# Kernel tuning notes

Measured on AMD Instinct MI355X. Metric: run time of the kernel, lower is better.

The kernel has to match this reference:

```python
import jax, jax.numpy as jnp
import numpy as np
import math

B, Q, K, C, H, D = 2, 2048, 2048, 512, 8, 64  # hidden_dim*num_heads == C


def setup_inputs() -> dict:
    key = jax.random.key(0)
    ks = jax.random.split(key, 9)
    s = 0.02
    return {
        "query_data": jax.random.normal(ks[0], (B, Q, C), jnp.float32),
        "key_data": jax.random.normal(ks[1], (B, K, C), jnp.float32),
        "bias1": jax.random.normal(ks[2], (B, 1, Q, K), jnp.float32),
        "bias2": jax.random.normal(ks[3], (1, H, Q, K), jnp.float32),
        "wq": jax.random.normal(ks[4], (C, H * D), jnp.float32) * s,
        "wk": jax.random.normal(ks[5], (C, H * D), jnp.float32) * s,
        "wv": jax.random.normal(ks[6], (C, H * D), jnp.float32) * s,
        "wo": jax.random.normal(ks[7], (H * D, C), jnp.float32) * s,
        "bo": jnp.zeros((C,), jnp.float32),
        "wg": jax.random.normal(ks[8], (C, H * D), jnp.float32) * s,
        "bg": jnp.zeros((H * D,), jnp.float32),
    }


def reference(query_data, key_data, bias1, bias2, wq, wk, wv, wo, bo, wg, bg):
    # prep_qkv: project, split heads, scale q by 1/sqrt(hidden_dim)
    q = (query_data @ wq).reshape(B, Q, H, D) / math.sqrt(D)
    k = (key_data @ wk).reshape(B, K, H, D)
    v = (key_data @ wv).reshape(B, K, H, D)
    # attention: scores [B,H,Q,K] with additive biases, softmax over K
    scores = jnp.einsum("bqhd,bkhd->bhqk", q, k) + bias1 + bias2
    attn = jax.nn.softmax(scores, axis=-1)
    out = jnp.einsum("bhqk,bkhd->bqhd", attn, v)  # [B,Q,H,D]
    # wrap_up: sigmoid gate from query data, flatten heads, output proj
    g = jax.nn.sigmoid(query_data @ wg + bg).reshape(B, Q, H, D)
    out = (out * g).reshape(B, Q, H * D)
    return out @ wo + bo
```

## Files before the change

### kernel.cpp

```cpp
#include <hip/hip_runtime.h>

typedef __bf16 bf16;
typedef __bf16 bf16x8 __attribute__((ext_vector_type(8)));
typedef __bf16 bf16x4 __attribute__((ext_vector_type(4)));
typedef float f32x4 __attribute__((ext_vector_type(4)));

#define NB 2
#define NQ 2048
#define NKK 2048
#define NC 512
#define NH 8
#define ND 64
#define NM (NB*NQ)
#define SPLITS 4
#define KSPL (NKK/SPLITS)
#define NTILES (KSPL/32)

__global__ __launch_bounds__(256) void cvt_bf16_kernel(const float* __restrict__ in,
                                                       bf16* __restrict__ out, int n4) {
  int i = blockIdx.x * 256 + threadIdx.x;
  if (i < n4) {
    float4 v = ((const float4*)in)[i];
    bf16x4 o;
    o[0] = (bf16)v.x; o[1] = (bf16)v.y; o[2] = (bf16)v.z; o[3] = (bf16)v.w;
    ((bf16x4*)out)[i] = o;
  }
}

__global__ __launch_bounds__(256) void transpose_w_kernel(const float* __restrict__ W,
                                                          bf16* __restrict__ WT) {
  __shared__ float t[32][33];
  int n0 = blockIdx.x * 32, k0 = blockIdx.y * 32;
  int c = threadIdx.x & 31, r0 = threadIdx.x >> 5;
  for (int r = r0; r < 32; r += 8) t[r][c] = W[(size_t)(k0 + r) * NC + n0 + c];
  __syncthreads();
  for (int r = r0; r < 32; r += 8) WT[(size_t)(n0 + r) * NC + k0 + c] = (bf16)t[c][r];
}

__global__ __launch_bounds__(256) void gemm_kernel(const bf16* __restrict__ X,
                                                   const bf16* __restrict__ WT,
                                                   const float* __restrict__ bias,
                                                   void* __restrict__ out, int epi) {
  __shared__ bf16 Xs[64][72];
  __shared__ bf16 Ws[64][72];
  int m0 = blockIdx.y * 64, n0 = blockIdx.x * 64;
  int tid = threadIdx.x, lane = tid & 63, wave = tid >> 6;
  int wm = wave >> 1, wn = wave & 1;
  int lr = lane & 15, lg = lane >> 4;
  f32x4 acc[2][2] = {};
  for (int k0 = 0; k0 < 512; k0 += 64) {
#pragma unroll
    for (int j = 0; j < 2; j++) {
      int cc = tid + 256 * j;
      int r = cc >> 3, c8 = (cc & 7) * 8;
      *(uint4*)&Xs[r][c8] = *(const uint4*)&X[(size_t)(m0 + r) * 512 + k0 + c8];
      *(uint4*)&Ws[r][c8] = *(const uint4*)&WT[(size_t)(n0 + r) * 512 + k0 + c8];
    }
    __syncthreads();
#pragma unroll
    for (int kk = 0; kk < 64; kk += 32) {
      bf16x8 a[2], b[2];
      a[0] = *(const bf16x8*)&Xs[wm * 32 + lr][kk + lg * 8];
      a[1] = *(const bf16x8*)&Xs[wm * 32 + 16 + lr][kk + lg * 8];
      b[0] = *(const bf16x8*)&Ws[wn * 32 + lr][kk + lg * 8];
      b[1] = *(const bf16x8*)&Ws[wn * 32 + 16 + lr][kk + lg * 8];
#pragma unroll
      for (int mi = 0; mi < 2; mi++)
#pragma unroll
        for (int ni = 0; ni < 2; ni++)
          acc[mi][ni] = __builtin_amdgcn_mfma_f32_16x16x32_bf16(a[mi], b[ni], acc[mi][ni], 0, 0, 0);
    }
    __syncthreads();
  }
#pragma unroll
  for (int mi = 0; mi < 2; mi++) {
#pragma unroll
    for (int ni = 0; ni < 2; ni++) {
#pragma unroll
      for (int i = 0; i < 4; i++) {
        int grow = m0 + wm * 32 + mi * 16 + lg * 4 + i;
        int gcol = n0 + wn * 32 + ni * 16 + lr;
        float v = acc[mi][ni][i];
        if (epi == 0) {
          int b = grow >> 11, q = grow & 2047, h = gcol >> 6, d = gcol & 63;
          ((bf16*)out)[((size_t)(b * NH + h) * NQ + q) * ND + d] = (bf16)(v * 0.125f);
        } else if (epi == 1 || epi == 2) {
          int b = grow >> 11, kq = grow & 2047, h = gcol >> 6, d = gcol & 63;
          ((bf16*)out)[((size_t)(b * NH + h) * NKK + kq) * ND + d] = (bf16)v;
        } else if (epi == 3) {
          v += bias[gcol];
          v = 1.0f / (1.0f + __expf(-v));
          ((float*)out)[(size_t)grow * 512 + gcol] = v;
        } else {
          ((float*)out)[(size_t)grow * 512 + gcol] = v + bias[gcol];
        }
      }
    }
  }
}

__global__ __launch_bounds__(256) void transpose_v_kernel(const bf16* __restrict__ vh,
                                                          bf16* __restrict__ vT) {
  __shared__ bf16 t[64][72];
  int bh = blockIdx.y;
  int kk0 = blockIdx.x * 64;
  const bf16* src = vh + (size_t)bh * NKK * ND;
  bf16* dst = vT + (size_t)bh * ND * NKK;
#pragma unroll
  for (int j = 0; j < 2; j++) {
    int c = threadIdx.x + 256 * j;
    int r = c >> 3, cc = (c & 7) * 8;
    *(uint4*)&t[r][cc] = *(const uint4*)&src[(size_t)(kk0 + r) * ND + cc];
  }
  __syncthreads();
#pragma unroll
  for (int j = 0; j < 2; j++) {
    int c = threadIdx.x + 256 * j;
    int d = c >> 3, ck = (c & 7) * 8;
    bf16 tmp[8];
#pragma unroll
    for (int x = 0; x < 8; x++) tmp[x] = t[ck + x][d];
    *(uint4*)&dst[(size_t)d * NKK + kk0 + ck] = *(const uint4*)tmp;
  }
}

struct Tile {
  float b1v[2][4];
  float b2v[2][4];
  bf16x8 kf[2][2];
  bf16x8 vf[4];
};

__device__ __forceinline__ void load_tile(int k0, const float* __restrict__ b1,
                                          const float* __restrict__ b2,
                                          const bf16* __restrict__ Kp,
                                          const bf16* __restrict__ Vt,
                                          int lr, int lg, Tile& T) {
#pragma unroll
  for (int f = 0; f < 2; f++) {
#pragma unroll
    for (int i = 0; i < 4; i++) {
      int row = lg * 4 + i;
      int col = k0 + f * 16 + lr;
      T.b1v[f][i] = b1[row * NKK + col];
      T.b2v[f][i] = b2[row * NKK + col];
    }
  }
#pragma unroll
  for (int f = 0; f < 2; f++) {
#pragma unroll
    for (int kc = 0; kc < 2; kc++)
      T.kf[f][kc] = *(const bf16x8*)&Kp[(size_t)(k0 + f * 16 + lr) * ND + kc * 32 + lg * 8];
  }
#pragma unroll
  for (int ni = 0; ni < 4; ni++)
    T.vf[ni] = *(const bf16x8*)&Vt[(size_t)(ni * 16 + lr) * NKK + k0 + lg * 8];
}

__device__ __forceinline__ void compute_tile(const Tile& T, bf16x8 qf0, bf16x8 qf1,
                                             f32x4 (&o)[4], float (&lrow)[4],
                                             bf16 (*pl)[36], int lr, int lg) {
  f32x4 s[2];
#pragma unroll
  for (int f = 0; f < 2; f++) {
    f32x4 c;
#pragma unroll
    for (int i = 0; i < 4; i++) c[i] = T.b1v[f][i] + T.b2v[f][i];
    c = __builtin_amdgcn_mfma_f32_16x16x32_bf16(qf0, T.kf[f][0], c, 0, 0, 0);
    c = __builtin_amdgcn_mfma_f32_16x16x32_bf16(qf1, T.kf[f][1], c, 0, 0, 0);
    s[f] = c;
  }
#pragma unroll
  for (int i = 0; i < 4; i++) {
    float p0 = __expf(s[0][i]);
    float p1 = __expf(s[1][i]);
    lrow[i] += p0 + p1;
    pl[lg * 4 + i][lr] = (bf16)p0;
    pl[lg * 4 + i][16 + lr] = (bf16)p1;
  }
  bf16x8 pa = *(const bf16x8*)&pl[lr][lg * 8];
#pragma unroll
  for (int ni = 0; ni < 4; ni++)
    o[ni] = __builtin_amdgcn_mfma_f32_16x16x32_bf16(pa, T.vf[ni], o[ni], 0, 0, 0);
}

__global__ __launch_bounds__(1024, 4) void attn_kernel(
    const bf16* __restrict__ qh, const bf16* __restrict__ kh, const bf16* __restrict__ vT,
    const float* __restrict__ bias1, const float* __restrict__ bias2,
    float* __restrict__ o_part, float* __restrict__ l_part) {
  __shared__ bf16 plds[16][16][36];
  int l = blockIdx.x;
  int swz = (l & 7) * 64 + (l >> 3);
  int q0 = (swz & 127) * 16;
  int split = swz >> 7;
  int w = threadIdx.x >> 6, lane = threadIdx.x & 63;
  int b = w >> 3, h = w & 7;
  int lr = lane & 15, lg = lane >> 4;
  int kbase = split * KSPL;
  const bf16* Qp = qh + ((size_t)(b * NH + h) * NQ + q0) * ND;
  const bf16* Kp = kh + (size_t)(b * NH + h) * NKK * ND;
  const bf16* Vt = vT + (size_t)(b * NH + h) * ND * NKK;
  const float* b1 = bias1 + ((size_t)b * NQ + q0) * NKK;
  const float* b2 = bias2 + ((size_t)h * NQ + q0) * NKK;

  bf16x8 qf0 = *(const bf16x8*)&Qp[lr * 64 + lg * 8];
  bf16x8 qf1 = *(const bf16x8*)&Qp[lr * 64 + 32 + lg * 8];

  f32x4 o[4] = {};
  float lrow[4] = {0.f, 0.f, 0.f, 0.f};
  bf16(*pl)[36] = plds[w];

  Tile T;
  for (int t = 0; t < NTILES; t++) {
    load_tile(kbase + t * 32, b1, b2, Kp, Vt, lr, lg, T);
    compute_tile(T, qf0, qf1, o, lrow, pl, lr, lg);
  }

  float lred[4];
#pragma unroll
  for (int i = 0; i < 4; i++) {
    float L = lrow[i];
    L += __shfl_xor(L, 1);
    L += __shfl_xor(L, 2);
    L += __shfl_xor(L, 4);
    L += __shfl_xor(L, 8);
    lred[i] = L;
  }

  float* op = o_part + (((size_t)(split * NB + b) * NH + h) * NQ + q0) * ND;
#pragma unroll
  for (int ni = 0; ni < 4; ni++)
#pragma unroll
    for (int i = 0; i < 4; i++)
      op[(lg * 4 + i) * ND + ni * 16 + lr] = o[ni][i];
  if (lr == 0) {
    float* lp = l_part + ((size_t)(split * NB + b) * NH + h) * NQ + q0;
#pragma unroll
    for (int i = 0; i < 4; i++) lp[lg * 4 + i] = lred[i];
  }
}

__global__ __launch_bounds__(256) void combine_kernel(const float* __restrict__ o_part,
                                                      const float* __restrict__ l_part,
                                                      const float* __restrict__ gate,
                                                      bf16* __restrict__ ao) {
  size_t t = (size_t)blockIdx.x * 256 + threadIdx.x;
  int d0 = (int)(t & 15) * 4;
  int h = (int)((t >> 4) & 7);
  int q = (int)((t >> 7) & 2047);
  int b = (int)(t >> 18);
  f32x4 acc = {};
  float L = 0.f;
#pragma unroll
  for (int s = 0; s < SPLITS; s++) {
    size_t base = (((size_t)(s * NB + b) * NH + h) * NQ + q);
    acc += *(const f32x4*)&o_part[base * ND + d0];
    L += l_part[base];
  }
  float inv = 1.0f / L;
  size_t gi = ((size_t)b * NQ + q) * 512 + h * 64 + d0;
  f32x4 g = *(const f32x4*)&gate[gi];
  bf16x4 r;
#pragma unroll
  for (int j = 0; j < 4; j++) r[j] = (bf16)(acc[j] * inv * g[j]);
  *(bf16x4*)&ao[gi] = r;
}

extern "C" void kernel_launch(void* const* d_in, const int* in_sizes, int n_in,
                              void* d_out, int out_size, void* d_ws, size_t ws_size,
                              hipStream_t stream) {
  const float* query = (const float*)d_in[0];
  const float* keyd  = (const float*)d_in[1];
  const float* bias1 = (const float*)d_in[2];
  const float* bias2 = (const float*)d_in[3];
  const float* wq = (const float*)d_in[4];
  const float* wk = (const float*)d_in[5];
  const float* wv = (const float*)d_in[6];
  const float* wo = (const float*)d_in[7];
  const float* bo = (const float*)d_in[8];
  const float* wg = (const float*)d_in[9];
  const float* bg = (const float*)d_in[10];

  char* ws = (char*)d_ws;
  size_t off = 0;
  auto alloc = [&](size_t bytes) {
    void* p = ws + off;
    off += (bytes + 255) & ~(size_t)255;
    return p;
  };
  bf16* qd_bf = (bf16*)alloc((size_t)NM * 512 * 2);
  bf16* kd_bf = (bf16*)alloc((size_t)NM * 512 * 2);
  bf16* wqT = (bf16*)alloc((size_t)512 * 512 * 2);
  bf16* wkT = (bf16*)alloc((size_t)512 * 512 * 2);
  bf16* wvT = (bf16*)alloc((size_t)512 * 512 * 2);
  bf16* wgT = (bf16*)alloc((size_t)512 * 512 * 2);
  bf16* woT = (bf16*)alloc((size_t)512 * 512 * 2);
  bf16* qh  = (bf16*)alloc((size_t)NB * NH * NQ * ND * 2);
  bf16* kh  = (bf16*)alloc((size_t)NB * NH * NKK * ND * 2);
  bf16* vh  = (bf16*)alloc((size_t)NB * NH * NKK * ND * 2);
  bf16* vTt = (bf16*)alloc((size_t)NB * NH * ND * NKK * 2);
  float* gbuf = (float*)alloc((size_t)NM * 512 * 4);
  bf16* aob = (bf16*)alloc((size_t)NM * 512 * 2);
  float* o_part = (float*)alloc((size_t)SPLITS * NB * NH * NQ * ND * 4);
  float* l_part = (float*)alloc((size_t)SPLITS * NB * NH * NQ * 4);

  int n4 = NM * 512 / 4;
  cvt_bf16_kernel<<<dim3(n4 / 256), 256, 0, stream>>>(query, qd_bf, n4);
  cvt_bf16_kernel<<<dim3(n4 / 256), 256, 0, stream>>>(keyd, kd_bf, n4);

  transpose_w_kernel<<<dim3(16, 16), 256, 0, stream>>>(wq, wqT);
  transpose_w_kernel<<<dim3(16, 16), 256, 0, stream>>>(wk, wkT);
  transpose_w_kernel<<<dim3(16, 16), 256, 0, stream>>>(wv, wvT);
  transpose_w_kernel<<<dim3(16, 16), 256, 0, stream>>>(wg, wgT);
  transpose_w_kernel<<<dim3(16, 16), 256, 0, stream>>>(wo, woT);

  gemm_kernel<<<dim3(8, 64), 256, 0, stream>>>(qd_bf, wqT, nullptr, qh, 0);
  gemm_kernel<<<dim3(8, 64), 256, 0, stream>>>(kd_bf, wkT, nullptr, kh, 1);
  gemm_kernel<<<dim3(8, 64), 256, 0, stream>>>(kd_bf, wvT, nullptr, vh, 2);
  gemm_kernel<<<dim3(8, 64), 256, 0, stream>>>(qd_bf, wgT, bg, gbuf, 3);

  transpose_v_kernel<<<dim3(32, 16), 256, 0, stream>>>(vh, vTt);

  attn_kernel<<<dim3(512), 1024, 0, stream>>>(qh, kh, vTt, bias1, bias2, o_part, l_part);

  combine_kernel<<<dim3((NB * NQ * NH * 16) / 256), 256, 0, stream>>>(o_part, l_part, gbuf, aob);

  gemm_kernel<<<dim3(8, 64), 256, 0, stream>>>(aob, woT, bo, d_out, 4);
}
```

Baseline: 258.7 us.

## Transpose QK^T mfma so bias loads vectorize, and prefetch bias tiles ahead

Swaps the operands of the score MFMA so each lane holds four consecutive key columns for one query row. The bias1/bias2 reads then become 16-byte float4 loads instead of scattered scalar loads. Bias tiles are double-buffered one tile ahead in a fully unrolled loop. The probability writes to LDS become packed bf16x4 stores with a padded stride of 40, and the row-sum reduction shrinks to two shuffles. Register pressure rises from the unrolling and prefetch, which could hurt occupancy at the 1024-thread launch bound.

```diff
diff --git a/kernel.cpp b/kernel.cpp
--- a/kernel.cpp
+++ b/kernel.cpp
@@ -15,6 +15,7 @@
 #define SPLITS 4
 #define KSPL (NKK/SPLITS)
 #define NTILES (KSPL/32)
+#define PLS 40
 
 __global__ __launch_bounds__(256) void cvt_bf16_kernel(const float* __restrict__ in,
                                                        bf16* __restrict__ out, int n4) {
@@ -124,71 +125,11 @@
   }
 }
 
-struct Tile {
-  float b1v[2][4];
-  float b2v[2][4];
-  bf16x8 kf[2][2];
-  bf16x8 vf[4];
-};
-
-__device__ __forceinline__ void load_tile(int k0, const float* __restrict__ b1,
-                                          const float* __restrict__ b2,
-                                          const bf16* __restrict__ Kp,
-                                          const bf16* __restrict__ Vt,
-                                          int lr, int lg, Tile& T) {
-#pragma unroll
-  for (int f = 0; f < 2; f++) {
-#pragma unroll
-    for (int i = 0; i < 4; i++) {
-      int row = lg * 4 + i;
-      int col = k0 + f * 16 + lr;
-      T.b1v[f][i] = b1[row * NKK + col];
-      T.b2v[f][i] = b2[row * NKK + col];
-    }
-  }
-#pragma unroll
-  for (int f = 0; f < 2; f++) {
-#pragma unroll
-    for (int kc = 0; kc < 2; kc++)
-      T.kf[f][kc] = *(const bf16x8*)&Kp[(size_t)(k0 + f * 16 + lr) * ND + kc * 32 + lg * 8];
-  }
-#pragma unroll
-  for (int ni = 0; ni < 4; ni++)
-    T.vf[ni] = *(const bf16x8*)&Vt[(size_t)(ni * 16 + lr) * NKK + k0 + lg * 8];
-}
-
-__device__ __forceinline__ void compute_tile(const Tile& T, bf16x8 qf0, bf16x8 qf1,
-                                             f32x4 (&o)[4], float (&lrow)[4],
-                                             bf16 (*pl)[36], int lr, int lg) {
-  f32x4 s[2];
-#pragma unroll
-  for (int f = 0; f < 2; f++) {
-    f32x4 c;
-#pragma unroll
-    for (int i = 0; i < 4; i++) c[i] = T.b1v[f][i] + T.b2v[f][i];
-    c = __builtin_amdgcn_mfma_f32_16x16x32_bf16(qf0, T.kf[f][0], c, 0, 0, 0);
-    c = __builtin_amdgcn_mfma_f32_16x16x32_bf16(qf1, T.kf[f][1], c, 0, 0, 0);
-    s[f] = c;
-  }
-#pragma unroll
-  for (int i = 0; i < 4; i++) {
-    float p0 = __expf(s[0][i]);
-    float p1 = __expf(s[1][i]);
-    lrow[i] += p0 + p1;
-    pl[lg * 4 + i][lr] = (bf16)p0;
-    pl[lg * 4 + i][16 + lr] = (bf16)p1;
-  }
-  bf16x8 pa = *(const bf16x8*)&pl[lr][lg * 8];
-#pragma unroll
-  for (int ni = 0; ni < 4; ni++)
-    o[ni] = __builtin_amdgcn_mfma_f32_16x16x32_bf16(pa, T.vf[ni], o[ni], 0, 0, 0);
-}
-
 __global__ __launch_bounds__(1024, 4) void attn_kernel(
     const bf16* __restrict__ qh, const bf16* __restrict__ kh, const bf16* __restrict__ vT,
     const float* __restrict__ bias1, const float* __restrict__ bias2,
     float* __restrict__ o_part, float* __restrict__ l_part) {
-  __shared__ bf16 plds[16][16][36];
+  __shared__ bf16 plds[16][16][PLS];
   int l = blockIdx.x;
   int swz = (l & 7) * 64 + (l >> 3);
   int q0 = (swz & 127) * 16;
@@ -198,34 +139,75 @@
   int lr = lane & 15, lg = lane >> 4;
   int kbase = split * KSPL;
   const bf16* Qp = qh + ((size_t)(b * NH + h) * NQ + q0) * ND;
-  const bf16* Kp = kh + (size_t)(b * NH + h) * NKK * ND;
-  const bf16* Vt = vT + (size_t)(b * NH + h) * ND * NKK;
-  const float* b1 = bias1 + ((size_t)b * NQ + q0) * NKK;
-  const float* b2 = bias2 + ((size_t)h * NQ + q0) * NKK;
+  const bf16* Kp = kh + (size_t)(b * NH + h) * NKK * ND + (size_t)kbase * ND;
+  const bf16* Vt = vT + (size_t)(b * NH + h) * ND * NKK + kbase;
+  const float* b1p = bias1 + ((size_t)b * NQ + q0 + lr) * NKK + kbase + lg * 4;
+  const float* b2p = bias2 + ((size_t)h * NQ + q0 + lr) * NKK + kbase + lg * 4;
 
   bf16x8 qf0 = *(const bf16x8*)&Qp[lr * 64 + lg * 8];
   bf16x8 qf1 = *(const bf16x8*)&Qp[lr * 64 + 32 + lg * 8];
 
   f32x4 o[4] = {};
-  float lrow[4] = {0.f, 0.f, 0.f, 0.f};
-  bf16(*pl)[36] = plds[w];
-
-  Tile T;
-  for (int t = 0; t < NTILES; t++) {
-    load_tile(kbase + t * 32, b1, b2, Kp, Vt, lr, lg, T);
-    compute_tile(T, qf0, qf1, o, lrow, pl, lr, lg);
-  }
-
-  float lred[4];
-#pragma unroll
-  for (int i = 0; i < 4; i++) {
-    float L = lrow[i];
-    L += __shfl_xor(L, 1);
-    L += __shfl_xor(L, 2);
-    L += __shfl_xor(L, 4);
-    L += __shfl_xor(L, 8);
-    lred[i] = L;
-  }
+  float lsum = 0.f;
+  bf16(*pl)[PLS] = plds[w];
+
+  f32x4 b1A0, b1A1, b2A0, b2A1, b1B0, b1B1, b2B0, b2B1;
+
+#define LOAD_BIAS(kt, b1lo, b1hi, b2lo, b2hi)              \
+  do {                                                     \
+    const float* p1 = b1p + (kt) * 32;                     \
+    const float* p2 = b2p + (kt) * 32;                     \
+    b1lo = *(const f32x4*)p1;  b1hi = *(const f32x4*)(p1 + 16); \
+    b2lo = *(const f32x4*)p2;  b2hi = *(const f32x4*)(p2 + 16); \
+  } while (0)
+
+#define COMPUTE(kt, b1lo, b1hi, b2lo, b2hi)                                        \
+  do {                                                                             \
+    const bf16* kp = Kp + (size_t)((kt) * 32 + lr) * ND + lg * 8;                  \
+    bf16x8 kf00 = *(const bf16x8*)kp;                                              \
+    bf16x8 kf01 = *(const bf16x8*)(kp + 32);                                       \
+    bf16x8 kf10 = *(const bf16x8*)(kp + 16 * ND);                                  \
+    bf16x8 kf11 = *(const bf16x8*)(kp + 16 * ND + 32);                             \
+    bf16x8 vf0 = *(const bf16x8*)&Vt[(size_t)(0 * 16 + lr) * NKK + (kt) * 32 + lg * 8]; \
+    bf16x8 vf1 = *(const bf16x8*)&Vt[(size_t)(1 * 16 + lr) * NKK + (kt) * 32 + lg * 8]; \
+    bf16x8 vf2 = *(const bf16x8*)&Vt[(size_t)(2 * 16 + lr) * NKK + (kt) * 32 + lg * 8]; \
+    bf16x8 vf3 = *(const bf16x8*)&Vt[(size_t)(3 * 16 + lr) * NKK + (kt) * 32 + lg * 8]; \
+    f32x4 c0 = {}, c1 = {};                                                        \
+    c0 = __builtin_amdgcn_mfma_f32_16x16x32_bf16(kf00, qf0, c0, 0, 0, 0);          \
+    c0 = __builtin_amdgcn_mfma_f32_16x16x32_bf16(kf01, qf1, c0, 0, 0, 0);          \
+    c1 = __builtin_amdgcn_mfma_f32_16x16x32_bf16(kf10, qf0, c1, 0, 0, 0);          \
+    c1 = __builtin_amdgcn_mfma_f32_16x16x32_bf16(kf11, qf1, c1, 0, 0, 0);          \
+    bf16x4 pk0, pk1;                                                               \
+    _Pragma("unroll")                                                              \
+    for (int i = 0; i < 4; i++) {                                                  \
+      float p0 = __expf(c0[i] + b1lo[i] + b2lo[i]);                                \
+      float p1v = __expf(c1[i] + b1hi[i] + b2hi[i]);                               \
+      lsum += p0 + p1v;                                                            \
+      pk0[i] = (bf16)p0;  pk1[i] = (bf16)p1v;                                      \
+    }                                                                              \
+    *(bf16x4*)&pl[lr][lg * 4] = pk0;                                               \
+    *(bf16x4*)&pl[lr][16 + lg * 4] = pk1;                                          \
+    bf16x8 pa = *(const bf16x8*)&pl[lr][lg * 8];                                   \
+    o[0] = __builtin_amdgcn_mfma_f32_16x16x32_bf16(pa, vf0, o[0], 0, 0, 0);        \
+    o[1] = __builtin_amdgcn_mfma_f32_16x16x32_bf16(pa, vf1, o[1], 0, 0, 0);        \
+    o[2] = __builtin_amdgcn_mfma_f32_16x16x32_bf16(pa, vf2, o[2], 0, 0, 0);        \
+    o[3] = __builtin_amdgcn_mfma_f32_16x16x32_bf16(pa, vf3, o[3], 0, 0, 0);        \
+  } while (0)
+
+  LOAD_BIAS(0, b1A0, b1A1, b2A0, b2A1);
+#pragma unroll
+  for (int t = 0; t < NTILES; t += 2) {
+    LOAD_BIAS(t + 1, b1B0, b1B1, b2B0, b2B1);
+    COMPUTE(t, b1A0, b1A1, b2A0, b2A1);
+    if (t + 2 < NTILES) LOAD_BIAS(t + 2, b1A0, b1A1, b2A0, b2A1);
+    COMPUTE(t + 1, b1B0, b1B1, b2B0, b2B1);
+  }
+#undef LOAD_BIAS
+#undef COMPUTE
+
+  float L = lsum;
+  L += __shfl_xor(L, 16);
+  L += __shfl_xor(L, 32);
 
   float* op = o_part + (((size_t)(split * NB + b) * NH + h) * NQ + q0) * ND;
 #pragma unroll
@@ -233,10 +215,9 @@
 #pragma unroll
     for (int i = 0; i < 4; i++)
       op[(lg * 4 + i) * ND + ni * 16 + lr] = o[ni][i];
-  if (lr == 0) {
+  if (lg == 0) {
     float* lp = l_part + ((size_t)(split * NB + b) * NH + h) * NQ + q0;
-#pragma unroll
-    for (int i = 0; i < 4; i++) lp[lg * 4 + i] = lred[i];
+    lp[lr] = L;
   }
 }
 
```

Result: slower. 290.7 us (+12.3%).
